# Kernel tuning notes

Hardware: AMD Instinct MI355X
Metric: run time of the kernel (lower is better)

The kernel has to match this reference:

```python
import jax, jax.numpy as jnp
import numpy as np

D = 1024      # embed_dim
H = 16        # attention heads
DH = D // H   # head size
B, S = 8, 1024
EPS = 1e-5


def setup_inputs() -> dict:
    key = jax.random.key(0)
    ks = jax.random.split(key, 12)
    s = lambda fan: 1.0 / np.sqrt(fan)
    return {
        "x":  jax.random.normal(ks[0], (B, S, D), dtype=jnp.float32),
        # per-head projections, stacked: [H, D, DH]
        "Wq": jax.random.normal(ks[1], (H, D, DH), jnp.float32) * s(D),
        "Wk": jax.random.normal(ks[2], (H, D, DH), jnp.float32) * s(D),
        "Wv": jax.random.normal(ks[3], (H, D, DH), jnp.float32) * s(D),
        "Wo": jax.random.normal(ks[4], (D, D), jnp.float32) * s(D),
        "bo": jnp.zeros((D,), jnp.float32),
        "g1": jnp.ones((D,), jnp.float32),
        "b1": jnp.zeros((D,), jnp.float32),
        "W1": jax.random.normal(ks[5], (D, 4 * D), jnp.float32) * s(D),
        "c1": jnp.zeros((4 * D,), jnp.float32),
        "W2": jax.random.normal(ks[6], (4 * D, D), jnp.float32) * s(4 * D),
        "c2": jnp.zeros((D,), jnp.float32),
        "g2": jnp.ones((D,), jnp.float32),
        "b2": jnp.zeros((D,), jnp.float32),
    }


def layer_norm(x, gain, bias):
    # torch uses unbiased variance (ddof=1)
    mean = jnp.mean(x, axis=-1, keepdims=True)
    var = jnp.var(x, axis=-1, keepdims=True, ddof=1)
    return (x - mean) / jnp.sqrt(var + EPS) * gain + bias


def reference(x, Wq, Wk, Wv, Wo, bo, g1, b1, W1, c1, W2, c2, g2, b2):
    # multi-head attention (all heads batched; same math as the per-head loop)
    q = jnp.einsum('bsd,hde->bhse', x, Wq)
    k = jnp.einsum('bsd,hde->bhse', x, Wk)
    v = jnp.einsum('bsd,hde->bhse', x, Wv)
    scores = jnp.einsum('bhse,bhte->bhst', q, k) / jnp.sqrt(jnp.float32(DH))
    attn = jax.nn.softmax(scores, axis=-1)
    ctx = jnp.einsum('bhst,bhte->bhse', attn, v)            # [B,H,S,DH]
    concat = ctx.transpose(0, 2, 1, 3).reshape(B, S, D)     # cat over heads
    attn_out = concat @ Wo + bo
    # residual + LN1
    h = layer_norm(x + attn_out, g1, b1)
    # FFN: Linear -> exact GELU -> Linear (torch nn.GELU default is erf form)
    ff = jax.nn.gelu(h @ W1 + c1, approximate=False) @ W2 + c2
    # residual + LN2
    return layer_norm(h + ff, g2, b2)
```

## Files before the change

kernel.cpp:

```cpp
#include <hip/hip_runtime.h>
#include <hip/hip_bf16.h>
#include <math.h>

typedef unsigned short u16;
typedef unsigned int u32;
typedef __attribute__((ext_vector_type(8))) __bf16 bf16x8;
typedef __attribute__((ext_vector_type(4))) float f32x4;
typedef __attribute__((ext_vector_type(16))) float f32x16;
typedef __attribute__((ext_vector_type(8))) u16 u16x8;
typedef __attribute__((ext_vector_type(4))) u16 u16x4;
typedef __attribute__((ext_vector_type(4))) u32 u32x4;

#define DEV static __device__ __forceinline__

DEV u16 f2bf(float x) {
  __bf16 b = (__bf16)x;
  return __builtin_bit_cast(u16, b);
}
DEV float bf2f(u16 u) {
  unsigned v = ((unsigned)u) << 16;
  return __builtin_bit_cast(float, v);
}

DEV void gl_lds16(const u16* g, u16* l) {
  __builtin_amdgcn_global_load_lds(
      (const __attribute__((address_space(1))) void*)g,
      (__attribute__((address_space(3))) void*)l, 16, 0, 0);
}

DEV float waveRedSum(float v) {
  v += __shfl_xor(v, 1);  v += __shfl_xor(v, 2);  v += __shfl_xor(v, 4);
  v += __shfl_xor(v, 8);  v += __shfl_xor(v, 16); v += __shfl_xor(v, 32);
  return v;
}

DEV float exp2_fast(float x) {
  float r;
  asm("v_exp_f32 %0, %1" : "=v"(r) : "v"(x));
  return r;
}
DEV float vmax16(f32x16 v) {
  float a = fmaxf(v[0], v[1]), b = fmaxf(v[2], v[3]);
  float c = fmaxf(v[4], v[5]), d = fmaxf(v[6], v[7]);
  float e = fmaxf(v[8], v[9]), f = fmaxf(v[10], v[11]);
  float g = fmaxf(v[12], v[13]), h = fmaxf(v[14], v[15]);
  a = fmaxf(a, b); c = fmaxf(c, d); e = fmaxf(e, f); g = fmaxf(g, h);
  return fmaxf(fmaxf(a, c), fmaxf(e, g));
}
DEV float vsum16(f32x16 v) {
  float a = v[0] + v[1], b = v[2] + v[3], c = v[4] + v[5], d = v[6] + v[7];
  float e = v[8] + v[9], f = v[10] + v[11], g = v[12] + v[13], h = v[14] + v[15];
  a += b; c += d; e += f; g += h;
  return (a + c) + (e + g);
}
DEV f32x16 mfma32(bf16x8 a, bf16x8 b, f32x16 c) {
  return __builtin_amdgcn_mfma_f32_32x32x16_bf16(a, b, c, 0, 0, 0);
}
DEV u32 pack2(float lo, float hi2) {
  return ((u32)f2bf(hi2) << 16) | (u32)f2bf(lo);
}
DEV void pack_direct(const f32x16& s, bf16x8* out) {
  u32x4 f0 = {pack2(s[0], s[1]),   pack2(s[2], s[3]),
              pack2(s[4], s[5]),   pack2(s[6], s[7])};
  u32x4 f1 = {pack2(s[8], s[9]),   pack2(s[10], s[11]),
              pack2(s[12], s[13]), pack2(s[14], s[15])};
  out[0] = __builtin_bit_cast(bf16x8, f0);
  out[1] = __builtin_bit_cast(bf16x8, f1);
}

__global__ __launch_bounds__(256)
void cvt_f32_bf16(const float* __restrict__ in, u16* __restrict__ out, int n8) {
  int i = blockIdx.x * 256 + threadIdx.x;
  if (i >= n8) return;
  const float4 a = *(const float4*)(in + (size_t)i * 8);
  const float4 b = *(const float4*)(in + (size_t)i * 8 + 4);
  u16x8 o;
  o[0] = f2bf(a.x); o[1] = f2bf(a.y); o[2] = f2bf(a.z); o[3] = f2bf(a.w);
  o[4] = f2bf(b.x); o[5] = f2bf(b.y); o[6] = f2bf(b.z); o[7] = f2bf(b.w);
  *(u16x8*)(out + (size_t)i * 8) = o;
}

__global__ __launch_bounds__(256)
void pack_wqkv(const float* __restrict__ Wq, const float* __restrict__ Wk,
               const float* __restrict__ Wv, u16* __restrict__ out) {
  __shared__ float tl[64][65];
  int bid = blockIdx.x;
  int which = bid / 256;
  int rem = bid % 256;
  int h = rem / 16, dt = rem % 16;
  const float* W = (which == 0) ? Wq : (which == 1) ? Wk : Wv;
  int t = threadIdx.x, tx = t & 63, ty = t >> 6;
  const float* src = W + (size_t)h * 65536 + (size_t)dt * 64 * 64;
#pragma unroll
  for (int i = 0; i < 16; ++i) {
    int dr = ty * 16 + i;
    tl[dr][tx] = src[(size_t)dr * 64 + tx];
  }
  __syncthreads();
#pragma unroll
  for (int i = 0; i < 16; ++i) {
    int e = ty * 16 + i;
    out[(size_t)(which * 1024 + h * 64 + e) * 1024 + dt * 64 + tx] = f2bf(tl[tx][e]);
  }
}

__global__ __launch_bounds__(256)
void pack_wt(const float* __restrict__ W, u16* __restrict__ out, int K, int N) {
  __shared__ float tl[64][65];
  int ntiles = N >> 6;
  int kt = blockIdx.x / ntiles, nt = blockIdx.x % ntiles;
  int t = threadIdx.x, tx = t & 63, ty = t >> 6;
#pragma unroll
  for (int i = 0; i < 16; ++i) {
    int kr = ty * 16 + i;
    tl[kr][tx] = W[(size_t)(kt * 64 + kr) * N + nt * 64 + tx];
  }
  __syncthreads();
#pragma unroll
  for (int i = 0; i < 16; ++i) {
    int nr = ty * 16 + i;
    out[(size_t)(nt * 64 + nr) * K + kt * 64 + tx] = f2bf(tl[tx][nr]);
  }
}

template <int EPI>
__global__ __launch_bounds__(256, 2)
void gemm_bt(const u16* __restrict__ A, const u16* __restrict__ Bt,
             void* __restrict__ Cout, const float* __restrict__ bias,
             int M, int N, int K,
             u16* __restrict__ qp_out, u16* __restrict__ kp_out,
             u16* __restrict__ vt_out) {
  __shared__ __align__(16) u16 As[128 * 32];
  __shared__ __align__(16) u16 Bs[128 * 32];
  const int t = threadIdx.x;
  const int lane = t & 63, w = t >> 6;
  const int li = lane & 15, lg = lane >> 4;
  const int tiles_n = N >> 7;
  const int nwg = gridDim.x;
  const int wgid = (blockIdx.x & 7) * (nwg >> 3) + (blockIdx.x >> 3);
  const int m0 = (wgid / tiles_n) << 7;
  const int n0 = (wgid % tiles_n) << 7;
  const int wm = (w >> 1) << 6, wn = (w & 1) << 6;

  f32x4 acc[4][4] = {};

  const int rowA = t >> 2, kcA = (t & 3) * 8;
  u16* aBase0 = &As[(size_t)(w * 64) * 8];
  u16* aBase1 = &As[(size_t)(256 + w * 64) * 8];
  u16* bBase0 = &Bs[(size_t)(w * 64) * 8];
  u16* bBase1 = &Bs[(size_t)(256 + w * 64) * 8];

  for (int k0 = 0; k0 < K; k0 += 32) {
    gl_lds16(A  + (size_t)(m0 + rowA) * K      + k0 + kcA, aBase0);
    gl_lds16(A  + (size_t)(m0 + 64 + rowA) * K + k0 + kcA, aBase1);
    gl_lds16(Bt + (size_t)(n0 + rowA) * K      + k0 + kcA, bBase0);
    gl_lds16(Bt + (size_t)(n0 + 64 + rowA) * K + k0 + kcA, bBase1);
    __syncthreads();
    bf16x8 af[4], bfr[4];
#pragma unroll
    for (int i = 0; i < 4; ++i)
      af[i] = *(const bf16x8*)&As[(wm + i * 16 + li) * 32 + lg * 8];
#pragma unroll
    for (int i = 0; i < 4; ++i)
      bfr[i] = *(const bf16x8*)&Bs[(wn + i * 16 + li) * 32 + lg * 8];
#pragma unroll
    for (int i = 0; i < 4; ++i)
#pragma unroll
      for (int j = 0; j < 4; ++j)
        acc[i][j] = __builtin_amdgcn_mfma_f32_16x16x32_bf16(af[i], bfr[j], acc[i][j], 0, 0, 0);
    __syncthreads();
  }

  if constexpr (EPI == 3) {
    const int which = n0 >> 10;
    const int colb = (n0 & 1023) + wn + li;
#pragma unroll
    for (int i = 0; i < 4; ++i) {
      const int row0 = m0 + wm + i * 16 + lg * 4;
      const int bb = row0 >> 10;
      const int s0r = row0 & 1023;
#pragma unroll
      for (int j = 0; j < 4; ++j) {
        const int c = colb + j * 16;
        const int hh = c >> 6, e = c & 63;
        const size_t hb = ((size_t)(bb * 16 + hh)) << 16;
        if (which == 2) {
          u16x4 pk;
#pragma unroll
          for (int r = 0; r < 4; ++r) pk[r] = f2bf(acc[i][j][r]);
          const int s_sw = (s0r & ~12) | ((s0r & 4) << 1) | ((s0r & 8) >> 1);
          *(u16x4*)(vt_out + hb + ((size_t)e << 10) + s_sw) = pk;
        } else {
          u16* dst = (which == 0) ? qp_out : kp_out;
#pragma unroll
          for (int r = 0; r < 4; ++r)
            dst[hb + (size_t)(s0r + r) * 64 + e] = f2bf(acc[i][j][r]);
        }
      }
    }
    return;
  }

  const int colBase = n0 + wn + li;
#pragma unroll
  for (int i = 0; i < 4; ++i) {
#pragma unroll
    for (int j = 0; j < 4; ++j) {
      int col = colBase + j * 16;
      float bv = (EPI >= 1) ? bias[col] : 0.0f;
#pragma unroll
      for (int r = 0; r < 4; ++r) {
        int row = m0 + wm + i * 16 + lg * 4 + r;
        float v = acc[i][j][r];
        if (EPI >= 1) v += bv;
        if (EPI == 2) v = 0.5f * v * (1.0f + erff(v * 0.70710678118654752f));
        if (EPI == 1) ((float*)Cout)[(size_t)row * N + col] = v;
        else          ((u16*)Cout)[(size_t)row * N + col] = f2bf(v);
      }
    }
  }
}

__global__ __launch_bounds__(256, 2)
void attn32(const u16* __restrict__ qp, const u16* __restrict__ kp,
            const u16* __restrict__ vt, u16* __restrict__ ctx) {
  __shared__ __align__(16) u16 lds[2][2][4096];
  const int t = threadIdx.x, l = t & 63, w = t >> 6;
  const int l31 = l & 31, hi = l >> 5;
  const int bid = blockIdx.x;
  const int idx = bid >> 3;
  const int bh = (bid & 7) * 16 + (idx >> 3);
  const int qt = idx & 7;
  const int b = bh >> 4, h = bh & 15;
  const int qg = qt * 128 + w * 32;
  const size_t base = (size_t)bh << 16;
  const float SC = 0.18033688011112042f;

  const u16* qrow = qp + base + (size_t)(qg + l31) * 64 + 8 * hi;
  bf16x8 qb[4];
#pragma unroll
  for (int f = 0; f < 4; ++f) qb[f] = *(const bf16x8*)(qrow + f * 16);

  const u16* kbh = kp + base;
  const u16* vbh = vt + base;

  const int sl0 = w, sl1 = 4 + w;

#define STAGE_KV(KB, BUF)                                                        \
  {                                                                              \
    u16* KT = &lds[BUF][0][0];                                                   \
    u16* VT = &lds[BUF][1][0];                                                   \
    const u16* ks = kbh + (size_t)(KB) * 4096;                                   \
    const u16* vs = vbh + (KB) * 64;                                             \
    gl_lds16(ks + (size_t)l * 64 + sl0 * 8,   KT + sl0 * 512);                   \
    gl_lds16(ks + (size_t)l * 64 + sl1 * 8,   KT + sl1 * 512);                   \
    gl_lds16(vs + (size_t)l * 1024 + sl0 * 8, VT + sl0 * 512);                   \
    gl_lds16(vs + (size_t)l * 1024 + sl1 * 8, VT + sl1 * 512);                   \
  }

  f32x16 o0 = {}, o1 = {};
  float m_run = -1e30f, l_run = 0.0f;

  STAGE_KV(0, 0);
  __syncthreads();

  int buf = 0;
  for (int kb = 0; kb < 16; ++kb) {
    if (kb < 15) STAGE_KV(kb + 1, buf ^ 1);

    const u16* KT = &lds[buf][0][0];
    const u16* VT = &lds[buf][1][0];

    bf16x8 ka[8];
#pragma unroll
    for (int f = 0; f < 4; ++f) {
      const int so = (2 * f + hi) * 512 + l31 * 8;
      ka[f]     = *(const bf16x8*)&KT[so];
      ka[4 + f] = *(const bf16x8*)&KT[so + 256];
    }

    __builtin_amdgcn_s_setprio(1);
    f32x16 s0 = {}, s1 = {};
#pragma unroll
    for (int f = 0; f < 4; ++f) s0 = mfma32(ka[f], qb[f], s0);
#pragma unroll
    for (int f = 0; f < 4; ++f) s1 = mfma32(ka[4 + f], qb[f], s1);
    __builtin_amdgcn_s_setprio(0);

    bf16x8 va[8];
#pragma unroll
    for (int c = 0; c < 4; ++c) {
      const int so = (2 * c + hi) * 512 + l31 * 8;
      va[c]     = *(const bf16x8*)&VT[so];
      va[4 + c] = *(const bf16x8*)&VT[so + 256];
    }

    s0 *= SC; s1 *= SC;

    float mx = fmaxf(vmax16(s0), vmax16(s1));
    mx = fmaxf(mx, __shfl_xor(mx, 32));

    float mn = fmaxf(m_run, mx);
    float al = exp2_fast(m_run - mn);
    m_run = mn;
    l_run *= al; o0 *= al; o1 *= al;

#pragma unroll
    for (int i = 0; i < 16; ++i) s0[i] = exp2_fast(s0[i] - m_run);
#pragma unroll
    for (int i = 0; i < 16; ++i) s1[i] = exp2_fast(s1[i] - m_run);

    float sm = vsum16(s0) + vsum16(s1);
    sm += __shfl_xor(sm, 32);
    l_run += sm;

    bf16x8 pb[4];
    pack_direct(s0, &pb[0]);
    pack_direct(s1, &pb[2]);

    __builtin_amdgcn_s_setprio(1);
    o0 = mfma32(va[0], pb[0], o0);
    o0 = mfma32(va[1], pb[1], o0);
    o0 = mfma32(va[2], pb[2], o0);
    o0 = mfma32(va[3], pb[3], o0);
    o1 = mfma32(va[4], pb[0], o1);
    o1 = mfma32(va[5], pb[1], o1);
    o1 = mfma32(va[6], pb[2], o1);
    o1 = mfma32(va[7], pb[3], o1);
    __builtin_amdgcn_s_setprio(0);

    __syncthreads();
    buf ^= 1;
  }
#undef STAGE_KV

  float inv = 1.0f / l_run;
  o0 *= inv; o1 *= inv;
  u16* crow = ctx + (size_t)(b * 1024 + qg + l31) * 1024 + h * 64 + 4 * hi;
#pragma unroll
  for (int g = 0; g < 4; ++g) {
    u16x4 p0, p1;
#pragma unroll
    for (int j = 0; j < 4; ++j) { p0[j] = f2bf(o0[g * 4 + j]); p1[j] = f2bf(o1[g * 4 + j]); }
    *(u16x4*)(crow + g * 8) = p0;
    *(u16x4*)(crow + 32 + g * 8) = p1;
  }
}

template <int MODE>
__global__ __launch_bounds__(256)
void ln_kernel(const void* __restrict__ in1v, const float* __restrict__ in2,
               const float* __restrict__ g, const float* __restrict__ bt,
               void* __restrict__ outv) {
  __shared__ float red[4];
  const int row = blockIdx.x;
  const int t = threadIdx.x;
  const int c = t * 4;
  const size_t base = (size_t)row * 1024 + c;

  float a0, a1, a2, a3;
  {
    const float4 y = *(const float4*)(in2 + base);
    if (MODE == 0) {
      const float4 x = *(const float4*)((const float*)in1v + base);
      a0 = x.x + y.x; a1 = x.y + y.y; a2 = x.z + y.z; a3 = x.w + y.w;
    } else {
      u16x4 xb = *(const u16x4*)((const u16*)in1v + base);
      a0 = bf2f(xb[0]) + y.x; a1 = bf2f(xb[1]) + y.y;
      a2 = bf2f(xb[2]) + y.z; a3 = bf2f(xb[3]) + y.w;
    }
  }
  float sum = waveRedSum(a0 + a1 + a2 + a3);
  if ((t & 63) == 0) red[t >> 6] = sum;
  __syncthreads();
  float mean = (red[0] + red[1] + red[2] + red[3]) * (1.0f / 1024.0f);
  __syncthreads();
  float d0 = a0 - mean, d1 = a1 - mean, d2 = a2 - mean, d3 = a3 - mean;
  float sq = waveRedSum(d0 * d0 + d1 * d1 + d2 * d2 + d3 * d3);
  if ((t & 63) == 0) red[t >> 6] = sq;
  __syncthreads();
  float var = (red[0] + red[1] + red[2] + red[3]) * (1.0f / 1023.0f);
  float inv = rsqrtf(var + 1e-5f);
  const float4 gv = *(const float4*)(g + c);
  const float4 bv = *(const float4*)(bt + c);
  float o0 = d0 * inv * gv.x + bv.x;
  float o1 = d1 * inv * gv.y + bv.y;
  float o2 = d2 * inv * gv.z + bv.z;
  float o3 = d3 * inv * gv.w + bv.w;
  if (MODE == 0) {
    u16x4 ob; ob[0] = f2bf(o0); ob[1] = f2bf(o1); ob[2] = f2bf(o2); ob[3] = f2bf(o3);
    *(u16x4*)((u16*)outv + base) = ob;
  } else {
    float4 of; of.x = o0; of.y = o1; of.z = o2; of.w = o3;
    *(float4*)((float*)outv + base) = of;
  }
}

extern "C" void kernel_launch(void* const* d_in, const int* in_sizes, int n_in,
                              void* d_out, int out_size, void* d_ws, size_t ws_size,
                              hipStream_t stream) {
  const float* x  = (const float*)d_in[0];
  const float* Wq = (const float*)d_in[1];
  const float* Wk = (const float*)d_in[2];
  const float* Wv = (const float*)d_in[3];
  const float* Wo = (const float*)d_in[4];
  const float* bo = (const float*)d_in[5];
  const float* g1 = (const float*)d_in[6];
  const float* b1 = (const float*)d_in[7];
  const float* W1 = (const float*)d_in[8];
  const float* c1 = (const float*)d_in[9];
  const float* W2 = (const float*)d_in[10];
  const float* c2 = (const float*)d_in[11];
  const float* g2 = (const float*)d_in[12];
  const float* b2 = (const float*)d_in[13];
  float* out = (float*)d_out;

  char* ws = (char*)d_ws;
  u16* xb     = (u16*)(ws + 0);
  u16* wqkv_b = (u16*)(ws + 16777216);
  u16* wo_b   = (u16*)(ws + 23068672);
  u16* w1_b   = (u16*)(ws + 25165824);
  u16* w2_b   = (u16*)(ws + 33554432);
  char* R1 = ws + 41943040;
  u16*  qpb  = (u16*)(R1);
  u16*  kpb  = (u16*)(R1 + 16777216);
  u16*  vtb  = (u16*)(R1 + 33554432);
  u16*  ctx  = (u16*)(R1 + 50331648);
  float* attn = (float*)(R1 + 67108864);
  u16*  ff1  = (u16*)(R1);
  float* ff2 = (float*)(R1 + 67108864);
  u16*  h_b  = xb;

  cvt_f32_bf16<<<4096, 256, 0, stream>>>(x, xb, 1048576);
  pack_wqkv<<<768, 256, 0, stream>>>(Wq, Wk, Wv, wqkv_b);
  pack_wt<<<256, 256, 0, stream>>>(Wo, wo_b, 1024, 1024);
  pack_wt<<<1024, 256, 0, stream>>>(W1, w1_b, 1024, 4096);
  pack_wt<<<1024, 256, 0, stream>>>(W2, w2_b, 4096, 1024);

  gemm_bt<3><<<64 * 24, 256, 0, stream>>>(xb, wqkv_b, nullptr, nullptr,
                                          8192, 3072, 1024, qpb, kpb, vtb);
  attn32<<<1024, 256, 0, stream>>>(qpb, kpb, vtb, ctx);
  gemm_bt<1><<<64 * 8, 256, 0, stream>>>(ctx, wo_b, attn, bo, 8192, 1024, 1024,
                                         nullptr, nullptr, nullptr);
  ln_kernel<0><<<8192, 256, 0, stream>>>(x, attn, g1, b1, h_b);
  gemm_bt<2><<<64 * 32, 256, 0, stream>>>(h_b, w1_b, ff1, c1, 8192, 4096, 1024,
                                          nullptr, nullptr, nullptr);
  gemm_bt<1><<<64 * 8, 256, 0, stream>>>(ff1, w2_b, ff2, c2, 8192, 1024, 4096,
                                         nullptr, nullptr, nullptr);
  ln_kernel<1><<<8192, 256, 0, stream>>>(h_b, ff2, g2, b2, out);
}
```

Baseline: 390.8 us.

## Replace GEMM with 256-wide tiles, 3-stage LDS pipeline and swizzled layout

Replaces the 128x128 single-buffered GEMM with a 512-thread kernel using 128x256 or 256x256 tiles, a triple-buffered global-to-LDS prefetch with explicit vmcnt waits, and an XOR-swizzled LDS layout to reduce bank conflicts. Larger tiles raise data reuse per load, and the prefetch overlaps memory with MFMA. The cost is more LDS and register pressure, and fewer workgroups (256 for the N=1024 GEMMs), which may underfill the 256 CUs.

Result: slower. 456.2 us (+16.8%).

```diff
diff --git a/kernel.cpp b/kernel.cpp
--- a/kernel.cpp
+++ b/kernel.cpp
@@ -123,60 +123,107 @@
   }
 }
 
-template <int EPI>
-__global__ __launch_bounds__(256, 2)
-void gemm_bt(const u16* __restrict__ A, const u16* __restrict__ Bt,
+template <int BM, int EPI>
+__global__ __launch_bounds__(512, 2)
+void gemm256(const u16* __restrict__ A, const u16* __restrict__ Bt,
              void* __restrict__ Cout, const float* __restrict__ bias,
              int M, int N, int K,
              u16* __restrict__ qp_out, u16* __restrict__ kp_out,
              u16* __restrict__ vt_out) {
-  __shared__ __align__(16) u16 As[128 * 32];
-  __shared__ __align__(16) u16 Bs[128 * 32];
+  constexpr int BN = 256;
+  constexpr int WT = BM / 2;
+  constexpr int FRW = WT / 16;
+  constexpr int SLOT = (BM + BN) * 32;
+  __shared__ __align__(16) u16 lds[3 * SLOT];
+
   const int t = threadIdx.x;
   const int lane = t & 63, w = t >> 6;
   const int li = lane & 15, lg = lane >> 4;
-  const int tiles_n = N >> 7;
+  const int wm = w >> 2, wn = w & 3;
+
+  const int tiles_n = N >> 8;
   const int nwg = gridDim.x;
   const int wgid = (blockIdx.x & 7) * (nwg >> 3) + (blockIdx.x >> 3);
-  const int m0 = (wgid / tiles_n) << 7;
-  const int n0 = (wgid % tiles_n) << 7;
-  const int wm = (w >> 1) << 6, wn = (w & 1) << 6;
-
-  f32x4 acc[4][4] = {};
-
-  const int rowA = t >> 2, kcA = (t & 3) * 8;
-  u16* aBase0 = &As[(size_t)(w * 64) * 8];
-  u16* aBase1 = &As[(size_t)(256 + w * 64) * 8];
-  u16* bBase0 = &Bs[(size_t)(w * 64) * 8];
-  u16* bBase1 = &Bs[(size_t)(256 + w * 64) * 8];
-
-  for (int k0 = 0; k0 < K; k0 += 32) {
-    gl_lds16(A  + (size_t)(m0 + rowA) * K      + k0 + kcA, aBase0);
-    gl_lds16(A  + (size_t)(m0 + 64 + rowA) * K + k0 + kcA, aBase1);
-    gl_lds16(Bt + (size_t)(n0 + rowA) * K      + k0 + kcA, bBase0);
-    gl_lds16(Bt + (size_t)(n0 + 64 + rowA) * K + k0 + kcA, bBase1);
+  const int m0 = (wgid / tiles_n) * BM;
+  const int n0 = (wgid % tiles_n) << 8;
+
+  const int srow = t >> 2;
+  const int scol = (((t & 3) ^ ((t >> 3) & 3)) << 3);
+  const u16* aS0 = A  + (size_t)(m0 + srow) * K + scol;
+  const u16* aS1 = A  + (size_t)(m0 + 128 + srow) * K + scol;
+  const u16* bS0 = Bt + (size_t)(n0 + srow) * K + scol;
+  const u16* bS1 = Bt + (size_t)(n0 + 128 + srow) * K + scol;
+  u16* dWave = &lds[w * 512];
+
+  int aOff[FRW], bOff[4];
+#pragma unroll
+  for (int i = 0; i < FRW; ++i) {
+    int row = wm * WT + i * 16 + li;
+    aOff[i] = row * 32 + ((lg ^ ((row >> 1) & 3)) << 3);
+  }
+#pragma unroll
+  for (int j = 0; j < 4; ++j) {
+    int row = wn * 64 + j * 16 + li;
+    bOff[j] = BM * 32 + row * 32 + ((lg ^ ((row >> 1) & 3)) << 3);
+  }
+
+  f32x4 acc[FRW][4] = {};
+  const int NT = K >> 5;
+
+#define STAGE256(TT, SL)                                             \
+  {                                                                  \
+    const int kk = (TT) << 5;                                        \
+    u16* db = dWave + (SL) * SLOT;                                   \
+    gl_lds16(aS0 + kk, db);                                          \
+    if constexpr (BM == 256) gl_lds16(aS1 + kk, db + 4096);          \
+    gl_lds16(bS0 + kk, db + BM * 32);                                \
+    gl_lds16(bS1 + kk, db + BM * 32 + 4096);                         \
+  }
+
+  STAGE256(0, 0);
+  STAGE256(1, 1);
+
+  int so = 0;
+  for (int tt = 0; tt < NT; ++tt) {
+    int s2 = so + 2; if (s2 >= 3) s2 -= 3;
+    if (tt + 2 < NT) {
+      STAGE256(tt + 2, s2);
+      if constexpr (BM == 256) asm volatile("s_waitcnt vmcnt(8)" ::: "memory");
+      else                     asm volatile("s_waitcnt vmcnt(6)" ::: "memory");
+    } else if (tt + 1 < NT) {
+      if constexpr (BM == 256) asm volatile("s_waitcnt vmcnt(4)" ::: "memory");
+      else                     asm volatile("s_waitcnt vmcnt(3)" ::: "memory");
+    } else {
+      asm volatile("s_waitcnt vmcnt(0)" ::: "memory");
+    }
     __syncthreads();
-    bf16x8 af[4], bfr[4];
-#pragma unroll
-    for (int i = 0; i < 4; ++i)
-      af[i] = *(const bf16x8*)&As[(wm + i * 16 + li) * 32 + lg * 8];
-#pragma unroll
-    for (int i = 0; i < 4; ++i)
-      bfr[i] = *(const bf16x8*)&Bs[(wn + i * 16 + li) * 32 + lg * 8];
-#pragma unroll
-    for (int i = 0; i < 4; ++i)
+
+    const u16* sb = &lds[so * SLOT];
+    bf16x8 af[FRW], bfr[4];
+#pragma unroll
+    for (int i = 0; i < FRW; ++i) af[i] = *(const bf16x8*)&sb[aOff[i]];
+#pragma unroll
+    for (int j = 0; j < 4; ++j) bfr[j] = *(const bf16x8*)&sb[bOff[j]];
+
+    __builtin_amdgcn_s_setprio(1);
+#pragma unroll
+    for (int i = 0; i < FRW; ++i)
 #pragma unroll
       for (int j = 0; j < 4; ++j)
         acc[i][j] = __builtin_amdgcn_mfma_f32_16x16x32_bf16(af[i], bfr[j], acc[i][j], 0, 0, 0);
+    __builtin_amdgcn_s_setprio(0);
+
     __syncthreads();
-  }
+    so = (so + 1 == 3) ? 0 : so + 1;
+  }
+#undef STAGE256
 
   if constexpr (EPI == 3) {
     const int which = n0 >> 10;
-    const int colb = (n0 & 1023) + wn + li;
-#pragma unroll
-    for (int i = 0; i < 4; ++i) {
-      const int row0 = m0 + wm + i * 16 + lg * 4;
+    const int colb = (n0 & 1023) + wn * 64 + li;
+#pragma unroll
+    for (int i = 0; i < FRW; ++i) {
+      const int row0 = m0 + wm * WT + i * 16 + lg * 4;
       const int bb = row0 >> 10;
       const int s0r = row0 & 1023;
 #pragma unroll
@@ -201,18 +248,17 @@
     return;
   }
 
-  const int colBase = n0 + wn + li;
-#pragma unroll
-  for (int i = 0; i < 4; ++i) {
+  const int colBase = n0 + wn * 64 + li;
+#pragma unroll
+  for (int i = 0; i < FRW; ++i) {
 #pragma unroll
     for (int j = 0; j < 4; ++j) {
       int col = colBase + j * 16;
-      float bv = (EPI >= 1) ? bias[col] : 0.0f;
+      float bv = bias[col];
 #pragma unroll
       for (int r = 0; r < 4; ++r) {
-        int row = m0 + wm + i * 16 + lg * 4 + r;
-        float v = acc[i][j][r];
-        if (EPI >= 1) v += bv;
+        int row = m0 + wm * WT + i * 16 + lg * 4 + r;
+        float v = acc[i][j][r] + bv;
         if (EPI == 2) v = 0.5f * v * (1.0f + erff(v * 0.70710678118654752f));
         if (EPI == 1) ((float*)Cout)[(size_t)row * N + col] = v;
         else          ((u16*)Cout)[(size_t)row * N + col] = f2bf(v);
@@ -243,7 +289,6 @@
 
   const u16* kbh = kp + base;
   const u16* vbh = vt + base;
-
   const int sl0 = w, sl1 = 4 + w;
 
 #define STAGE_KV(KB, BUF)                                                        \
@@ -274,9 +319,9 @@
     bf16x8 ka[8];
 #pragma unroll
     for (int f = 0; f < 4; ++f) {
-      const int so = (2 * f + hi) * 512 + l31 * 8;
-      ka[f]     = *(const bf16x8*)&KT[so];
-      ka[4 + f] = *(const bf16x8*)&KT[so + 256];
+      const int s = (2 * f + hi) * 512 + l31 * 8;
+      ka[f]     = *(const bf16x8*)&KT[s];
+      ka[4 + f] = *(const bf16x8*)&KT[s + 256];
     }
 
     __builtin_amdgcn_s_setprio(1);
@@ -290,9 +335,9 @@
     bf16x8 va[8];
 #pragma unroll
     for (int c = 0; c < 4; ++c) {
-      const int so = (2 * c + hi) * 512 + l31 * 8;
-      va[c]     = *(const bf16x8*)&VT[so];
-      va[4 + c] = *(const bf16x8*)&VT[so + 256];
+      const int s = (2 * c + hi) * 512 + l31 * 8;
+      va[c]     = *(const bf16x8*)&VT[s];
+      va[4 + c] = *(const bf16x8*)&VT[s + 256];
     }
 
     s0 *= SC; s1 *= SC;
@@ -437,15 +482,15 @@
   pack_wt<<<1024, 256, 0, stream>>>(W1, w1_b, 1024, 4096);
   pack_wt<<<1024, 256, 0, stream>>>(W2, w2_b, 4096, 1024);
 
-  gemm_bt<3><<<64 * 24, 256, 0, stream>>>(xb, wqkv_b, nullptr, nullptr,
-                                          8192, 3072, 1024, qpb, kpb, vtb);
+  gemm256<128, 3><<<768, 512, 0, stream>>>(xb, wqkv_b, nullptr, nullptr,
+                                           8192, 3072, 1024, qpb, kpb, vtb);
   attn32<<<1024, 256, 0, stream>>>(qpb, kpb, vtb, ctx);
-  gemm_bt<1><<<64 * 8, 256, 0, stream>>>(ctx, wo_b, attn, bo, 8192, 1024, 1024,
-                                         nullptr, nullptr, nullptr);
+  gemm256<128, 1><<<256, 512, 0, stream>>>(ctx, wo_b, attn, bo, 8192, 1024, 1024,
+                                           nullptr, nullptr, nullptr);
   ln_kernel<0><<<8192, 256, 0, stream>>>(x, attn, g1, b1, h_b);
-  gemm_bt<2><<<64 * 32, 256, 0, stream>>>(h_b, w1_b, ff1, c1, 8192, 4096, 1024,
-                                          nullptr, nullptr, nullptr);
-  gemm_bt<1><<<64 * 8, 256, 0, stream>>>(ff1, w2_b, ff2, c2, 8192, 1024, 4096,
-                                         nullptr, nullptr, nullptr);
+  gemm256<256, 2><<<512, 512, 0, stream>>>(h_b, w1_b, ff1, c1, 8192, 4096, 1024,
+                                           nullptr, nullptr, nullptr);
+  gemm256<128, 1><<<256, 512, 0, stream>>>(ff1, w2_b, ff2, c2, 8192, 1024, 4096,
+                                           nullptr, nullptr, nullptr);
   ln_kernel<1><<<8192, 256, 0, stream>>>(h_b, ff2, g2, b2, out);
 }
```
